# Kernel tuning notes

Measured on AMD Instinct MI355X. Metric: run time of the kernel, lower is better.

The kernel has to match this reference:

```python
import jax, jax.numpy as jnp
import numpy as np

N, E, D, B, C, K, L = 20000, 320000, 256, 16, 2, 6, 3
EPS = 1e-5
BETA, LAM = 0.3, 0.2
ALPHA = 1.0 - BETA - LAM


def setup_inputs() -> dict:
    key = jax.random.key(0)
    ks = jax.random.split(key, 32)
    s = 0.05
    inp = {
        "x": jax.random.normal(ks[0], (N, D), jnp.float32),
        "edge_index": jax.random.randint(ks[1], (2, E), 0, N, jnp.int64) if jax.config.jax_enable_x64 else jax.random.randint(ks[1], (2, E), 0, N, jnp.int32),
        "batch": jnp.sort(jax.random.randint(ks[2], (N,), 0, B, jnp.int32)),
        "labels": jax.random.randint(ks[3], (B,), 0, C, jnp.int32),
        # mask generator MLP: 2D -> 128 -> 64 -> 1
        "mw1": jax.random.normal(ks[4], (128, 2 * D), jnp.float32) * s,
        "mb1": jnp.zeros((128,), jnp.float32),
        "mw2": jax.random.normal(ks[5], (64, 128), jnp.float32) * s,
        "mb2": jnp.zeros((64,), jnp.float32),
        "mw3": jax.random.normal(ks[6], (1, 64), jnp.float32) * s,
        "mb3": jnp.zeros((1,), jnp.float32),
        # frozen CFG encoder: L DGCN layers (W_self, W_in, W_out + BN eval stats)
        "Ws": jax.random.normal(ks[7], (L, D, D), jnp.float32) * s,
        "bs": jnp.zeros((L, D), jnp.float32),
        "Win": jax.random.normal(ks[8], (L, D, D), jnp.float32) * s,
        "bin_": jnp.zeros((L, D), jnp.float32),
        "Wout": jax.random.normal(ks[9], (L, D, D), jnp.float32) * s,
        "bout": jnp.zeros((L, D), jnp.float32),
        "gamma": jnp.ones((L, D), jnp.float32),
        "beta": jnp.zeros((L, D), jnp.float32),
        "rmean": jax.random.normal(ks[10], (L, D), jnp.float32) * s,
        "rvar": jax.random.uniform(ks[11], (L, D), jnp.float32, 0.5, 1.5),
        # semantic anchors and frozen classifier
        "anchors": jax.random.normal(ks[12], (K, D), jnp.float32),
        "Wc": jax.random.normal(ks[13], (C, D), jnp.float32) * s,
        "bc": jnp.zeros((C,), jnp.float32),
    }
    return inp


def _encoder(x0, src, dst, mask, Ws, bs, Win, bin_, Wout, bout, gamma, beta, rmean, rvar):
    """Bidirectional edge-weighted gather/scatter_add message passing, L layers."""
    n = x0.shape[0]
    h = x0
    mcol = mask[:, None]
    for l in range(L):
        agg_in = jax.ops.segment_sum(h[src] * mcol, dst, num_segments=n)   # (N, D)
        agg_out = jax.ops.segment_sum(h[dst] * mcol, src, num_segments=n)  # (N, D)
        h = h @ Ws[l].T + bs[l] + agg_in @ Win[l].T + bin_[l] + agg_out @ Wout[l].T + bout[l]
        h = jax.nn.relu(h)
        h = (h - rmean[l]) * jax.lax.rsqrt(rvar[l] + EPS) * gamma[l] + beta[l]  # BN (eval)
    return h


def _anchor_stat(emb, anchors):
    # sum over anchors of euclidean distance: (B,)
    d = emb[:, None, :] - anchors[None, :, :]
    return jnp.sqrt(jnp.sum(d * d, axis=-1)).sum(axis=-1)


def reference(x, edge_index, batch, labels, mw1, mb1, mw2, mb2, mw3, mb3,
              Ws, bs, Win, bin_, Wout, bout, gamma, beta, rmean, rvar,
              anchors, Wc, bc):
    src, dst = edge_index[0], edge_index[1]
    enc = lambda m: _encoder(x, src, dst, m, Ws, bs, Win, bin_, Wout, bout, gamma, beta, rmean, rvar)

    ones_e = jnp.ones((src.shape[0],), x.dtype)
    node_emb = enc(ones_e)

    # mask generator: z = h_src || h_dst -> MLP -> sigmoid
    z = jnp.concatenate([node_emb[src], node_emb[dst]], axis=-1)  # (E, 2D)
    h1 = jax.nn.relu(z @ mw1.T + mb1)
    h2 = jax.nn.relu(h1 @ mw2.T + mb2)
    mask = jax.nn.sigmoid((h2 @ mw3.T + mb3)[:, 0])               # (E,)

    cnt = jnp.clip(jax.ops.segment_sum(jnp.ones((x.shape[0],), x.dtype), batch, num_segments=B), 1.0)

    def masked_fwd(m):
        h = enc(m)
        gemb = jax.ops.segment_sum(h, batch, num_segments=B) / cnt[:, None]  # mean pool
        return gemb @ Wc.T + bc, gemb

    logits_sub, emb_sub = masked_fwd(mask)
    logits_comp, _ = masked_fwd(1.0 - mask)
    _, orig_emb = masked_fwd(ones_e)
    orig_emb = jax.lax.stop_gradient(orig_emb)  # torch.no_grad() pass

    s_orig = _anchor_stat(orig_emb, anchors)
    s_sub = _anchor_stat(emb_sub, anchors)
    L_align = jnp.mean((s_sub - jax.lax.stop_gradient(s_orig)) ** 2)

    logp = jax.nn.log_softmax(logits_sub, axis=-1)
    L_pred = -jnp.mean(jnp.take_along_axis(logp, labels[:, None].astype(jnp.int32), axis=1)[:, 0])

    p_comp = jax.nn.softmax(logits_comp, axis=-1)
    u = 1.0 / C
    # F.kl_div(log(p+1e-8), uniform, 'batchmean')
    L_uni = jnp.sum(u * (jnp.log(u) - jnp.log(p_comp + 1e-8))) / B

    total = ALPHA * L_pred + BETA * L_uni + LAM * L_align
    return total, L_pred, L_uni, L_align, mask
```

## Files before the change

kernel.cpp:

```cpp
#include <hip/hip_runtime.h>
#include <hip/hip_bf16.h>

constexpr int Nn = 20000;
constexpr int Ee = 320000;
constexpr int Dd = 256;
constexpr int Bb = 16;
constexpr float EPSc = 1e-5f;

using v8s = __attribute__((ext_vector_type(8))) short;
using v4f = __attribute__((ext_vector_type(4))) float;
using v2f = __attribute__((ext_vector_type(2))) float;

__device__ __forceinline__ float b2f(ushort u) { return __uint_as_float(((unsigned)u) << 16); }
__device__ __forceinline__ ushort f2b(float f) {
  __hip_bfloat16 h = __float2bfloat16(f);
  return *reinterpret_cast<ushort*>(&h);
}

#ifndef __has_builtin
#define __has_builtin(x) 0
#endif
#if __has_builtin(__builtin_amdgcn_cvt_pk_f32_fp8) && __has_builtin(__builtin_amdgcn_cvt_pk_fp8_f32)
#define FP8CVT 1
#else
#define FP8CVT 0
#endif

__device__ __forceinline__ unsigned f2fp8(float v) {
#if FP8CVT
  return (unsigned)__builtin_amdgcn_cvt_pk_fp8_f32(v, 0.f, 0, false) & 0xFFu;
#else
  unsigned u = __float_as_uint(v);
  unsigned s = (u >> 24) & 0x80u;
  unsigned a = u & 0x7FFFFFFFu;
  if (a >= 0x43F00000u) return s | 0x7Eu;
  unsigned r = a + 0x0007FFFFu + ((a >> 20) & 1u);
  int e = (int)(r >> 23) - 120;
  if (e <= 0) return s;
  return s | ((unsigned)e << 3) | ((r >> 20) & 7u);
#endif
}

__device__ __forceinline__ void fp8x8_dec(unsigned lo, unsigned hi, float* f) {
#if FP8CVT
  v2f p0 = __builtin_amdgcn_cvt_pk_f32_fp8((int)lo, false);
  v2f p1 = __builtin_amdgcn_cvt_pk_f32_fp8((int)lo, true);
  v2f p2 = __builtin_amdgcn_cvt_pk_f32_fp8((int)hi, false);
  v2f p3 = __builtin_amdgcn_cvt_pk_f32_fp8((int)hi, true);
  f[0] = p0[0]; f[1] = p0[1]; f[2] = p1[0]; f[3] = p1[1];
  f[4] = p2[0]; f[5] = p2[1]; f[6] = p3[0]; f[7] = p3[1];
#else
#pragma unroll
  for (int j = 0; j < 8; ++j) {
    unsigned b = (j < 4) ? ((lo >> (8 * j)) & 0xFFu) : ((hi >> (8 * (j - 4))) & 0xFFu);
    unsigned s = (b & 0x80u) << 24;
    unsigned e = (b >> 3) & 15u, m = b & 7u;
    float x;
    if (e) x = __uint_as_float(s | ((e + 120u) << 23) | (m << 20));
    else { x = (float)(int)m * 0x1p-9f; if (s) x = -x; }
    f[j] = x;
  }
#endif
}

__global__ void hist_edges_k(const int* __restrict__ src, const int* __restrict__ dst,
                             int* __restrict__ cin, int* __restrict__ cout) {
  int e = blockIdx.x * 256 + threadIdx.x;
  if (e < Ee) { atomicAdd(&cin[dst[e]], 1); atomicAdd(&cout[src[e]], 1); }
}

__global__ void cnt_batch_k(const int* __restrict__ batch, float* __restrict__ cntf) {
  int b = threadIdx.x;
  if (b < Bb) {
    int lo = 0, hi = Nn;
    while (lo < hi) { int mid = (lo + hi) >> 1; if (batch[mid] < b) lo = mid + 1; else hi = mid; }
    int lb = lo;
    lo = 0; hi = Nn;
    while (lo < hi) { int mid = (lo + hi) >> 1; if (batch[mid] <= b) lo = mid + 1; else hi = mid; }
    cntf[b] = (float)(lo - lb);
  }
}

__global__ __launch_bounds__(1024) void scan_k(const int* __restrict__ cin,
                                               const int* __restrict__ cout,
                                               int* __restrict__ off_in, int* __restrict__ off_out,
                                               int* __restrict__ cur_in, int* __restrict__ cur_out) {
  __shared__ int part[1024];
  const int tid = threadIdx.x;
  for (int which = 0; which < 2; ++which) {
    const int* cnt = which ? cout : cin;
    int* off = which ? off_out : off_in;
    int* curp = which ? cur_out : cur_in;
    int vals[20];
    int base = tid * 20;
    int local = 0;
#pragma unroll
    for (int i = 0; i < 20; ++i) {
      int idx = base + i;
      int v = (idx < Nn) ? cnt[idx] : 0;
      vals[i] = v; local += v;
    }
    part[tid] = local;
    __syncthreads();
    for (int ofs = 1; ofs < 1024; ofs <<= 1) {
      int t = (tid >= ofs) ? part[tid - ofs] : 0;
      __syncthreads();
      part[tid] += t;
      __syncthreads();
    }
    int run = part[tid] - local;
#pragma unroll
    for (int i = 0; i < 20; ++i) {
      int idx = base + i;
      if (idx < Nn) { off[idx] = run; curp[idx] = run; run += vals[i]; }
    }
    if (tid == 0) off[Nn] = Ee;
    __syncthreads();
  }
}

__global__ void scatter_k(const int* __restrict__ src, const int* __restrict__ dst,
                          int* __restrict__ cur_in, int* __restrict__ cur_out,
                          int* __restrict__ in_src, int* __restrict__ in_eid,
                          int* __restrict__ out_dst, int* __restrict__ out_eid,
                          int* __restrict__ out_srcn) {
  int e = blockIdx.x * 256 + threadIdx.x;
  if (e < Ee) {
    int d = dst[e], s = src[e];
    int p = atomicAdd(&cur_in[d], 1);  in_src[p] = s;  in_eid[p] = e;
    int q = atomicAdd(&cur_out[s], 1); out_dst[q] = d; out_eid[q] = e; out_srcn[q] = s;
  }
}

__global__ void prep_bsum_k(const float* __restrict__ bs, const float* __restrict__ bin,
                            const float* __restrict__ bout, float* __restrict__ bsum) {
  int t = threadIdx.x;
  for (int l = 0; l < 3; ++l) bsum[l * 256 + t] = bs[l * 256 + t] + bin[l * 256 + t] + bout[l * 256 + t];
}

__global__ void copyxb_k(const float* __restrict__ x, ushort* __restrict__ h) {
  const int n4 = Nn * Dd / 4;
  int i = blockIdx.x * 256 + threadIdx.x;
  if (i < n4) {
    float4 v = ((const float4*)x)[i];
    ushort4 o; o.x = f2b(v.x); o.y = f2b(v.y); o.z = f2b(v.z); o.w = f2b(v.w);
    ((ushort4*)h)[i] = o;
  }
}

__global__ void c_f2b_k(const float* __restrict__ s, ushort* __restrict__ d, int n) {
  int i = blockIdx.x * 256 + threadIdx.x;
  if (i < n) d[i] = f2b(s[i]);
}

__global__ void prep_mlp_k(const float* __restrict__ mw1, const float* __restrict__ mb1,
                           const float* __restrict__ mw2,
                           ushort* __restrict__ Wcombb, ushort* __restrict__ W2b,
                           float* __restrict__ bcomb) {
  int i = blockIdx.x * 256 + threadIdx.x;
  if (i < 65536) {
    int r = i >> 8, c = i & 255;
    float v = (r < 128) ? mw1[r * 512 + c] : mw1[(r - 128) * 512 + 256 + c];
    Wcombb[i] = f2b(v);
  }
  if (i < 8192) W2b[i] = f2b(mw2[i]);
  if (i < 256) bcomb[i] = (i < 128) ? mb1[i] : 0.f;
}

__global__ void permmask_k(const float* __restrict__ mask,
                           const int* __restrict__ in_eid, float* __restrict__ minA) {
  int i = blockIdx.x * 256 + threadIdx.x;
  if (i < Ee) minA[i] = mask[in_eid[i]];
}

template <int EMIT8>
__global__ __launch_bounds__(256) void gemm768t_k(
    const ushort* __restrict__ A, const ushort* __restrict__ W0,
    const ushort* __restrict__ W1, const ushort* __restrict__ W2,
    ushort* __restrict__ Y, unsigned char* __restrict__ Y8, int M) {
  __shared__ ushort lds[10240];
  ushort* As = lds;
  ushort* Bs = lds + 5120;
  const int tid = threadIdx.x;
  const int wid = tid >> 6, lane = tid & 63;
  const int wr = wid & 1, wc = wid >> 1;
  const int m0 = blockIdx.x * 128;
  const int by = blockIdx.y;
  const int seg = by >> 1;
  const ushort* Wp = (seg == 0) ? W0 : ((seg == 1) ? W1 : W2);
  const int nb0 = (by & 1) * 128;
  const int lrow = lane & 15;
  const int klo = (lane >> 4) * 8;
  const int r0 = tid >> 2, c80 = (tid & 3) * 8;
  const int r1 = (tid + 256) >> 2, c81 = ((tid + 256) & 3) * 8;
  int ar0 = m0 + r0; if (ar0 >= M) ar0 = M - 1;
  int ar1 = m0 + r1; if (ar1 >= M) ar1 = M - 1;
  v4f acc[4][4] = {};
  for (int kc = 0; kc < 256; kc += 32) {
    __syncthreads();
    *(v8s*)&As[r0 * 40 + c80] = *(const v8s*)(A + (size_t)ar0 * 256 + kc + c80);
    *(v8s*)&As[r1 * 40 + c81] = *(const v8s*)(A + (size_t)ar1 * 256 + kc + c81);
    *(v8s*)&Bs[r0 * 40 + c80] = *(const v8s*)(Wp + (size_t)(nb0 + r0) * 256 + kc + c80);
    *(v8s*)&Bs[r1 * 40 + c81] = *(const v8s*)(Wp + (size_t)(nb0 + r1) * 256 + kc + c81);
    __syncthreads();
    v8s a[4], b[4];
#pragma unroll
    for (int f = 0; f < 4; ++f) {
      a[f] = *(const v8s*)&As[(wr * 64 + f * 16 + lrow) * 40 + klo];
      b[f] = *(const v8s*)&Bs[(wc * 64 + f * 16 + lrow) * 40 + klo];
    }
#pragma unroll
    for (int fi = 0; fi < 4; ++fi)
#pragma unroll
      for (int fj = 0; fj < 4; ++fj)
        acc[fi][fj] = __builtin_amdgcn_mfma_f32_16x16x32_bf16(a[fi], b[fj], acc[fi][fj], 0, 0, 0);
  }
  __syncthreads();
  const int colq = by * 128 + wc * 64;
  if (EMIT8) {
    unsigned char* ep = (unsigned char*)lds + wid * 3072;
#pragma unroll
    for (int hf = 0; hf < 2; ++hf) {
#pragma unroll
      for (int fi = 0; fi < 2; ++fi) {
        const int fI = hf * 2 + fi;
        const int rl0 = fi * 16 + ((lane >> 4) << 2);
#pragma unroll
        for (int fj = 0; fj < 4; ++fj)
#pragma unroll
          for (int r = 0; r < 4; ++r)
            ep[(rl0 + r) * 96 + fj * 16 + lrow] = (unsigned char)f2fp8(acc[fI][fj][r]);
      }
#pragma unroll
      for (int i = 0; i < 2; ++i) {
        const int rl = (lane >> 2) + i * 16;
        const int cb = (lane & 3) * 16;
        uint4 val = *(const uint4*)&ep[rl * 96 + cb];
        const int grow = m0 + wr * 64 + hf * 32 + rl;
        if (grow < M)
          *(uint4*)(Y8 + (size_t)grow * 768 + colq + cb) = val;
      }
    }
  } else {
    ushort* ep = lds + wid * 2304;
#pragma unroll
    for (int hf = 0; hf < 2; ++hf) {
#pragma unroll
      for (int fi = 0; fi < 2; ++fi) {
        const int fI = hf * 2 + fi;
        const int rl0 = fi * 16 + ((lane >> 4) << 2);
#pragma unroll
        for (int fj = 0; fj < 4; ++fj)
#pragma unroll
          for (int r = 0; r < 4; ++r)
            ep[(rl0 + r) * 72 + fj * 16 + lrow] = f2b(acc[fI][fj][r]);
      }
#pragma unroll
      for (int i = 0; i < 4; ++i) {
        const int rl = (lane >> 2) + (i & 1) * 16;
        const int oct = (lane & 3) + (i >> 1) * 4;
        v8s val = *(const v8s*)&ep[rl * 72 + oct * 8];
        const int grow = m0 + wr * 64 + hf * 32 + rl;
        if (grow < M)
          *(v8s*)(Y + (size_t)grow * 768 + colq + oct * 8) = val;
      }
    }
  }
}

template <int MODE, int WR>
__global__ __launch_bounds__(256) void aggepi_k(
    const ushort* __restrict__ Y, ushort* __restrict__ hout, ushort* __restrict__ raw,
    const int* __restrict__ off_in, const int* __restrict__ in_src,
    const int* __restrict__ off_out, const int* __restrict__ out_dst,
    const float* __restrict__ minA, const float* __restrict__ moutA,
    const float* __restrict__ bsum, const float* __restrict__ gma,
    const float* __restrict__ bta, const float* __restrict__ rmn, const float* __restrict__ rvr,
    int Mtot) {
  const int g = threadIdx.x >> 5;
  const int lane = threadIdx.x & 31;
  const int node = blockIdx.x * 8 + g;
  if (node >= Mtot) return;
  const int v = node;
  const int co = lane * 8;
  float acc[8] = {};
#pragma unroll
  for (int dir = 0; dir < 2; ++dir) {
    const int* offs = dir ? off_out : off_in;
    const int* nbr  = dir ? out_dst : in_src;
    const float* ma = dir ? moutA : minA;
    const ushort* Yg = Y + (dir ? 512 : 256) + co;
    const int s = offs[v], e = offs[v + 1];
    int i = s;
    for (; i + 4 <= e; i += 4) {
      int u[4]; float m[4];
#pragma unroll
      for (int t = 0; t < 4; ++t) {
        u[t] = nbr[i + t];
        m[t] = (MODE == 0) ? 1.f : ma[i + t];
      }
      v8s r[4];
#pragma unroll
      for (int t = 0; t < 4; ++t) r[t] = *(const v8s*)(Yg + (size_t)u[t] * 768);
#pragma unroll
      for (int t = 0; t < 4; ++t)
#pragma unroll
        for (int j = 0; j < 8; ++j) acc[j] += m[t] * b2f((ushort)r[t][j]);
    }
    for (; i < e; ++i) {
      int u = nbr[i];
      float m = (MODE == 0) ? 1.f : ma[i];
      v8s r = *(const v8s*)(Yg + (size_t)u * 768);
#pragma unroll
      for (int j = 0; j < 8; ++j) acc[j] += m * b2f((ushort)r[j]);
    }
  }
  if (WR) {
    v8s rw;
#pragma unroll
    for (int j = 0; j < 8; ++j) rw[j] = (short)f2b(acc[j]);
    *(v8s*)(raw + (size_t)v * 256 + co) = rw;
  }
  v8s ys = *(const v8s*)(Y + (size_t)v * 768 + co);
  v8s o;
#pragma unroll
  for (int j = 0; j < 8; ++j) {
    const int col = co + j;
    float val = acc[j] + b2f((ushort)ys[j]) + bsum[col];
    val = fmaxf(val, 0.f);
    val = (val - rmn[col]) * rsqrtf(rvr[col] + EPSc) * gma[col] + bta[col];
    o[j] = (short)f2b(val);
  }
  *(v8s*)(hout + (size_t)node * 256 + co) = o;
}

__global__ __launch_bounds__(256) void aggepi8_k(
    const unsigned char* __restrict__ Y8, ushort* __restrict__ hout,
    const int* __restrict__ off_in, const int* __restrict__ in_src,
    const int* __restrict__ off_out, const int* __restrict__ out_dst,
    const float* __restrict__ minA, const float* __restrict__ moutA,
    const float* __restrict__ bsum, const float* __restrict__ gma,
    const float* __restrict__ bta, const float* __restrict__ rmn, const float* __restrict__ rvr) {
  const int g = threadIdx.x >> 5;
  const int lane = threadIdx.x & 31;
  const int node = blockIdx.x * 8 + g;
  if (node >= 2 * Nn) return;
  const int half = (node >= Nn) ? 1 : 0;
  const int v = node - half * Nn;
  const int co = lane * 8;
  float acc[8] = {};
#pragma unroll
  for (int dir = 0; dir < 2; ++dir) {
    const int* offs = dir ? off_out : off_in;
    const int* nbr  = dir ? out_dst : in_src;
    const float* ma = dir ? moutA : minA;
    const unsigned char* Yg = Y8 + (size_t)half * Nn * 768 + (dir ? 512 : 256) + co;
    const int s = offs[v], e = offs[v + 1];
    int i = s;
    for (; i + 4 <= e; i += 4) {
      int u[4]; float m[4];
#pragma unroll
      for (int t = 0; t < 4; ++t) {
        u[t] = nbr[i + t];
        float mv = ma[i + t];
        m[t] = half ? (1.f - mv) : mv;
      }
      uint2 r[4];
#pragma unroll
      for (int t = 0; t < 4; ++t) r[t] = *(const uint2*)(Yg + (size_t)u[t] * 768);
#pragma unroll
      for (int t = 0; t < 4; ++t) {
        float f[8];
        fp8x8_dec(r[t].x, r[t].y, f);
#pragma unroll
        for (int j = 0; j < 8; ++j) acc[j] += m[t] * f[j];
      }
    }
    for (; i < e; ++i) {
      int u = nbr[i];
      float mv = ma[i];
      float m = half ? (1.f - mv) : mv;
      uint2 r = *(const uint2*)(Yg + (size_t)u * 768);
      float f[8];
      fp8x8_dec(r.x, r.y, f);
#pragma unroll
      for (int j = 0; j < 8; ++j) acc[j] += m * f[j];
    }
  }
  uint2 rs = *(const uint2*)(Y8 + (size_t)(half * Nn + v) * 768 + co);
  float fs[8];
  fp8x8_dec(rs.x, rs.y, fs);
  v8s o;
#pragma unroll
  for (int j = 0; j < 8; ++j) {
    const int col = co + j;
    float val = acc[j] + fs[j] + bsum[col];
    val = fmaxf(val, 0.f);
    val = (val - rmn[col]) * rsqrtf(rvr[col] + EPSc) * gma[col] + bta[col];
    o[j] = (short)f2b(val);
  }
  *(v8s*)(hout + (size_t)node * 256 + co) = o;
}

__global__ void compl0_k(const ushort* __restrict__ Yx, const ushort* __restrict__ Aones,
                         const ushort* __restrict__ Asub, ushort* __restrict__ hout,
                         const float* __restrict__ bsum, const float* __restrict__ gma,
                         const float* __restrict__ bta, const float* __restrict__ rmn,
                         const float* __restrict__ rvr) {
  int i = blockIdx.x * 256 + threadIdx.x;
  if (i >= Nn * 32) return;
  const int v = i >> 5;
  const int co = (i & 31) * 8;
  v8s ys = *(const v8s*)(Yx + (size_t)v * 768 + co);
  v8s ao = *(const v8s*)(Aones + (size_t)v * 256 + co);
  v8s as = *(const v8s*)(Asub + (size_t)v * 256 + co);
  v8s o;
#pragma unroll
  for (int j = 0; j < 8; ++j) {
    const int col = co + j;
    float val = b2f((ushort)ys[j]) + b2f((ushort)ao[j]) - b2f((ushort)as[j]) + bsum[col];
    val = fmaxf(val, 0.f);
    val = (val - rmn[col]) * rsqrtf(rvr[col] + EPSc) * gma[col] + bta[col];
    o[j] = (short)f2b(val);
  }
  *(v8s*)(hout + (size_t)(Nn + v) * 256 + co) = o;
}

template <int EPI>
__global__ __launch_bounds__(256) void mfma_gemm2_k(
    const ushort* __restrict__ A, const ushort* __restrict__ W,
    ushort* __restrict__ Cout, int M, const float* __restrict__ bias) {
  __shared__ ushort eplds[4][32][72];
  const int tid = threadIdx.x;
  const int wid = tid >> 6, lane = tid & 63;
  const int wr = wid & 1, wc = wid >> 1;
  const int m0 = blockIdx.x * 64 + wr * 32;
  const int n0 = blockIdx.y * 128 + wc * 64;
  const int lrow = lane & 15;
  const int klo = (lane >> 4) * 8;
  int rowA[2];
#pragma unroll
  for (int fi = 0; fi < 2; ++fi) {
    int r = m0 + fi * 16 + lrow;
    rowA[fi] = (r < M) ? r : (M - 1);
  }
  v4f acc[2][4] = {};
#pragma unroll
  for (int c = 0; c < 8; ++c) {
    v8s a[2], b[4];
#pragma unroll
    for (int fi = 0; fi < 2; ++fi)
      a[fi] = *(const v8s*)(A + (size_t)rowA[fi] * 256 + c * 32 + klo);
#pragma unroll
    for (int fj = 0; fj < 4; ++fj)
      b[fj] = *(const v8s*)(W + (size_t)(n0 + fj * 16 + lrow) * 256 + c * 32 + klo);
#pragma unroll
    for (int fi = 0; fi < 2; ++fi)
#pragma unroll
      for (int fj = 0; fj < 4; ++fj)
        acc[fi][fj] = __builtin_amdgcn_mfma_f32_16x16x32_bf16(a[fi], b[fj], acc[fi][fj], 0, 0, 0);
  }
#pragma unroll
  for (int fj = 0; fj < 4; ++fj) {
    const int col = n0 + fj * 16 + lrow;
    const float bsv = bias ? bias[col] : 0.f;
#pragma unroll
    for (int fi = 0; fi < 2; ++fi) {
      const int rl0 = fi * 16 + ((lane >> 4) << 2);
#pragma unroll
      for (int r = 0; r < 4; ++r)
        eplds[wid][rl0 + r][fj * 16 + lrow] = f2b(acc[fi][fj][r] + bsv);
    }
  }
#pragma unroll
  for (int i = 0; i < 4; ++i) {
    const int rl = (lane >> 2) + (i & 1) * 16;
    const int oct = (lane & 3) + (i >> 1) * 4;
    v8s val = *(const v8s*)&eplds[wid][rl][oct * 8];
    const int grow = m0 + rl;
    if (grow < M)
      *(v8s*)(Cout + (size_t)grow * 256 + n0 + oct * 8) = val;
  }
}

__global__ __launch_bounds__(256) void edge_mlp4_k(const ushort* __restrict__ P,
                                                   const int* __restrict__ out_srcn,
                                                   const int* __restrict__ out_dst,
                                                   const int* __restrict__ out_eid,
                                                   const ushort* __restrict__ W2b,
                                                   const float* __restrict__ b2, const float* __restrict__ w3,
                                                   const float* __restrict__ b3,
                                                   float* __restrict__ maskOut, float* __restrict__ moutA) {
  const int tid = threadIdx.x;
  const int w = tid >> 6, lane = tid & 63;
  const int e0 = blockIdx.x * 64 + w * 16;
  const int le = lane & 15;
  const int kq = lane >> 4;
  const int klo = kq * 8;
  const int pA = e0 + le;
  const int s_ = out_srcn[pA], d_ = out_dst[pA];
  const ushort* ps = P + (size_t)s_ * 256;
  const ushort* pd = P + (size_t)d_ * 256 + 128;
  v8s as[4], ad[4];
#pragma unroll
  for (int c = 0; c < 4; ++c) {
    as[c] = *(const v8s*)(ps + c * 32 + klo);
    ad[c] = *(const v8s*)(pd + c * 32 + klo);
  }
  v4f acc[4] = {};
#pragma unroll
  for (int c = 0; c < 4; ++c) {
    v8s h;
#pragma unroll
    for (int j = 0; j < 8; ++j) {
      float v = fmaxf(b2f((ushort)as[c][j]) + b2f((ushort)ad[c][j]), 0.f);
      h[j] = (short)f2b(v);
    }
#pragma unroll
    for (int fj = 0; fj < 4; ++fj) {
      v8s b = *(const v8s*)(W2b + (size_t)(fj * 16 + le) * 128 + c * 32 + klo);
      acc[fj] = __builtin_amdgcn_mfma_f32_16x16x32_bf16(h, b, acc[fj], 0, 0, 0);
    }
  }
  float b2v[4], w3v[4];
#pragma unroll
  for (int fj = 0; fj < 4; ++fj) { b2v[fj] = b2[fj * 16 + le]; w3v[fj] = w3[fj * 16 + le]; }
  const float b3v = b3[0];
#pragma unroll
  for (int r = 0; r < 4; ++r) {
    float val = 0.f;
#pragma unroll
    for (int fj = 0; fj < 4; ++fj)
      val += fmaxf(acc[fj][r] + b2v[fj], 0.f) * w3v[fj];
    val += __shfl_xor(val, 1);
    val += __shfl_xor(val, 2);
    val += __shfl_xor(val, 4);
    val += __shfl_xor(val, 8);
    if (le == 0) {
      int pos = e0 + kq * 4 + r;
      float sig = 1.0f / (1.0f + expf(-(val + b3v)));
      moutA[pos] = sig;
      maskOut[out_eid[pos]] = sig;
    }
  }
}

__global__ __launch_bounds__(256) void gemb_sum_k(const ushort* __restrict__ h, const int* __restrict__ batch,
                                                  float* __restrict__ gsum, int batched) {
  const int halfBlocks = Nn / 16;
  int blk = blockIdx.x;
  int half = 0, bi = blk;
  if (batched) { half = (blk >= halfBlocks) ? 1 : 0; bi = blk - half * halfBlocks; }
  const int v0 = bi * 16;
  const int tid = threadIdx.x;
  const size_t base = (size_t)half * Nn;
  float* out = gsum + (size_t)half * (Bb * Dd);
  float acc = 0.0f;
  int curb = batch[v0];
  for (int i = 0; i < 16; ++i) {
    int v = v0 + i;
    int b = batch[v];
    if (b != curb) { atomicAdd(&out[curb * Dd + tid], acc); acc = 0.0f; curb = b; }
    acc += b2f(h[(base + v) * Dd + tid]);
  }
  atomicAdd(&out[curb * Dd + tid], acc);
}

__global__ void gemb_scale_k(float* __restrict__ g, const float* __restrict__ cntf) {
  int blk = blockIdx.x;
  int b = blk & 15;
  g[blk * Dd + threadIdx.x] /= fmaxf(cntf[b], 1.0f);
}

__global__ void anchor_k(const float* __restrict__ g, const float* __restrict__ anchors,
                         float* __restrict__ s_out) {
  __shared__ float red4[4];
  const int b = blockIdx.x, tid = threadIdx.x;
  float gv = g[b * Dd + tid];
  float total = 0.0f;
  for (int k = 0; k < 6; ++k) {
    float d = gv - anchors[k * Dd + tid];
    float v = d * d;
    for (int o = 32; o > 0; o >>= 1) v += __shfl_xor(v, o);
    if ((tid & 63) == 0) red4[tid >> 6] = v;
    __syncthreads();
    if (tid == 0) total += sqrtf(red4[0] + red4[1] + red4[2] + red4[3]);
    __syncthreads();
  }
  if (tid == 0) s_out[b] = total;
}

__global__ void logits_k(const float* __restrict__ gsub, const float* __restrict__ gcomp,
                         const float* __restrict__ Wc, const float* __restrict__ bc,
                         float* __restrict__ outL) {
  __shared__ float red4[4];
  const int blk = blockIdx.x;
  const int set = blk >> 4, b = blk & 15;
  const float* g = set ? gcomp : gsub;
  const int tid = threadIdx.x;
  float gv = g[b * Dd + tid];
  for (int c = 0; c < 2; ++c) {
    float v = gv * Wc[c * Dd + tid];
    for (int o = 32; o > 0; o >>= 1) v += __shfl_xor(v, o);
    if ((tid & 63) == 0) red4[tid >> 6] = v;
    __syncthreads();
    if (tid == 0) outL[set * 32 + b * 2 + c] = red4[0] + red4[1] + red4[2] + red4[3] + bc[c];
    __syncthreads();
  }
}

__global__ void final_k(const float* __restrict__ L, const int* __restrict__ labels,
                        const float* __restrict__ s_orig, const float* __restrict__ s_sub,
                        float* __restrict__ out) {
  if (threadIdx.x == 0) {
    float Lp = 0, Lu = 0, La = 0;
    const float u = 0.5f;
    for (int b = 0; b < 16; ++b) {
      float l0 = L[b * 2], l1 = L[b * 2 + 1];
      float m = fmaxf(l0, l1);
      float lse = m + logf(expf(l0 - m) + expf(l1 - m));
      int lab = labels[b];
      Lp += -((lab ? l1 : l0) - lse);
      float c0 = L[32 + b * 2], c1 = L[32 + b * 2 + 1];
      float mm = fmaxf(c0, c1);
      float e0 = expf(c0 - mm), e1 = expf(c1 - mm), Z = e0 + e1;
      Lu += u * (logf(u) - logf(e0 / Z + 1e-8f)) + u * (logf(u) - logf(e1 / Z + 1e-8f));
      float dd = s_sub[b] - s_orig[b];
      La += dd * dd;
    }
    Lp /= 16.0f; Lu /= 16.0f; La /= 16.0f;
    out[0] = 0.5f * Lp + 0.3f * Lu + 0.2f * La;
    out[1] = Lp; out[2] = Lu; out[3] = La;
  }
}

extern "C" void kernel_launch(void* const* d_in, const int* in_sizes, int n_in,
                              void* d_out, int out_size, void* d_ws, size_t ws_size,
                              hipStream_t stream) {
  (void)in_sizes; (void)n_in; (void)out_size; (void)ws_size;
  const float* x    = (const float*)d_in[0];
  const int* ei     = (const int*)d_in[1];
  const int* batch  = (const int*)d_in[2];
  const int* labels = (const int*)d_in[3];
  const float* mw1 = (const float*)d_in[4];
  const float* mb1 = (const float*)d_in[5];
  const float* mw2 = (const float*)d_in[6];
  const float* mb2 = (const float*)d_in[7];
  const float* mw3 = (const float*)d_in[8];
  const float* mb3 = (const float*)d_in[9];
  const float* Ws   = (const float*)d_in[10];
  const float* bs   = (const float*)d_in[11];
  const float* Win  = (const float*)d_in[12];
  const float* bin_ = (const float*)d_in[13];
  const float* Wout = (const float*)d_in[14];
  const float* bout = (const float*)d_in[15];
  const float* gma  = (const float*)d_in[16];
  const float* bta  = (const float*)d_in[17];
  const float* rmn  = (const float*)d_in[18];
  const float* rvr  = (const float*)d_in[19];
  const float* anchors = (const float*)d_in[20];
  const float* Wc   = (const float*)d_in[21];
  const float* bc   = (const float*)d_in[22];
  const int* srcp = ei;
  const int* dstp = ei + Ee;

  const size_t NH = (size_t)Nn * Dd;
  const size_t NY = (size_t)Nn * 768;
  ushort* xb   = (ushort*)d_ws;
  ushort* hA   = xb + NH;
  ushort* hB   = hA + 2 * NH;
  ushort* Yx   = hB + 2 * NH;
  ushort* Ybuf = Yx + NY;
  ushort* Pb   = Ybuf;
  unsigned char* Y8 = (unsigned char*)Ybuf;
  ushort* Aones = Ybuf + 2 * NY;
  ushort* Asub  = Aones + NH;
  ushort* Wsb   = Asub + NH;
  ushort* Winb  = Wsb + 3 * 65536;
  ushort* Woutb = Winb + 3 * 65536;
  ushort* Wcombb = Woutb + 3 * 65536;
  ushort* W2b    = Wcombb + 65536;
  float* bcomb = (float*)(W2b + 8192);
  float* minA  = bcomb + 256;
  float* moutA = minA + Ee;
  int* off_in   = (int*)(moutA + Ee);
  int* off_out  = off_in + (Nn + 1);
  int* cur_in   = off_out + (Nn + 1);
  int* cur_out  = cur_in + Nn;
  int* in_src   = cur_out + Nn;
  int* in_eid   = in_src + Ee;
  int* out_dst  = in_eid + Ee;
  int* out_eid  = out_dst + Ee;
  int* out_srcn = out_eid + Ee;
  int* counts_in  = out_srcn + Ee;
  int* counts_out = counts_in + Nn;
  float* cntf      = (float*)(counts_out + Nn);
  float* gemb_orig = cntf + Bb;
  float* gemb_sub  = gemb_orig + Bb * Dd;
  float* gemb_comp = gemb_sub + Bb * Dd;
  float* bsum    = gemb_comp + Bb * Dd;
  float* s_orig  = bsum + 3 * Dd;
  float* s_sub   = s_orig + Bb;
  float* logitsb = s_sub + Bb;

  float* outF = (float*)d_out;
  float* maskp = outF + 4;

  const size_t zero_bytes = (char*)bsum - (char*)counts_in;
  hipMemsetAsync(counts_in, 0, zero_bytes, stream);

  hist_edges_k<<<(Ee + 255) / 256, 256, 0, stream>>>(srcp, dstp, counts_in, counts_out);
  cnt_batch_k<<<1, 64, 0, stream>>>(batch, cntf);
  scan_k<<<1, 1024, 0, stream>>>(counts_in, counts_out, off_in, off_out, cur_in, cur_out);
  scatter_k<<<(Ee + 255) / 256, 256, 0, stream>>>(srcp, dstp, cur_in, cur_out, in_src, in_eid,
                                                  out_dst, out_eid, out_srcn);
  prep_bsum_k<<<1, 256, 0, stream>>>(bs, bin_, bout, bsum);

  c_f2b_k<<<(3 * 65536 + 255) / 256, 256, 0, stream>>>(Ws, Wsb, 3 * 65536);
  c_f2b_k<<<(3 * 65536 + 255) / 256, 256, 0, stream>>>(Win, Winb, 3 * 65536);
  c_f2b_k<<<(3 * 65536 + 255) / 256, 256, 0, stream>>>(Wout, Woutb, 3 * 65536);
  prep_mlp_k<<<256, 256, 0, stream>>>(mw1, mb1, mw2, Wcombb, W2b, bcomb);

  auto run_gemm768 = [&](const ushort* h, ushort* Yout, int M, int l) {
    dim3 gg((M + 127) / 128, 6);
    gemm768t_k<0><<<gg, 256, 0, stream>>>(h, Wsb + (size_t)l * 65536, Winb + (size_t)l * 65536,
                                          Woutb + (size_t)l * 65536, Yout, nullptr, M);
  };
  auto run_gemm768_8 = [&](const ushort* h, int M, int l) {
    dim3 gg((M + 127) / 128, 6);
    gemm768t_k<1><<<gg, 256, 0, stream>>>(h, Wsb + (size_t)l * 65536, Winb + (size_t)l * 65536,
                                          Woutb + (size_t)l * 65536, nullptr, Y8, M);
  };
  auto bn = [&](int l) { return bsum + l * 256; };
  const int aggN = (Nn + 7) / 8;
  const int agg2N = (2 * Nn + 7) / 8;

  copyxb_k<<<(Nn * Dd / 4 + 255) / 256, 256, 0, stream>>>(x, xb);
  run_gemm768(xb, Yx, Nn, 0);
  aggepi_k<0, 1><<<aggN, 256, 0, stream>>>(
      Yx, hB, Aones, off_in, in_src, off_out, out_dst, nullptr, nullptr,
      bn(0), gma, bta, rmn, rvr, Nn);
  run_gemm768(hB, Ybuf, Nn, 1);
  aggepi_k<0, 0><<<aggN, 256, 0, stream>>>(
      Ybuf, hA, nullptr, off_in, in_src, off_out, out_dst, nullptr, nullptr,
      bn(1), gma + 256, bta + 256, rmn + 256, rvr + 256, Nn);
  run_gemm768(hA, Ybuf, Nn, 2);
  aggepi_k<0, 0><<<aggN, 256, 0, stream>>>(
      Ybuf, hB, nullptr, off_in, in_src, off_out, out_dst, nullptr, nullptr,
      bn(2), gma + 512, bta + 512, rmn + 512, rvr + 512, Nn);

  gemb_sum_k<<<Nn / 16, 256, 0, stream>>>(hB, batch, gemb_orig, 0);
  gemb_scale_k<<<Bb, 256, 0, stream>>>(gemb_orig, cntf);
  anchor_k<<<Bb, 256, 0, stream>>>(gemb_orig, anchors, s_orig);

  {
    dim3 gp((Nn + 63) / 64, 2);
    mfma_gemm2_k<3><<<gp, 256, 0, stream>>>(hB, Wcombb, Pb, Nn, bcomb);
  }
  edge_mlp4_k<<<Ee / 64, 256, 0, stream>>>(Pb, out_srcn, out_dst, out_eid,
                                           W2b, mb2, mw3, mb3, maskp, moutA);
  permmask_k<<<(Ee + 255) / 256, 256, 0, stream>>>(maskp, in_eid, minA);

  aggepi_k<1, 1><<<aggN, 256, 0, stream>>>(
      Yx, hA, Asub, off_in, in_src, off_out, out_dst, minA, moutA,
      bn(0), gma, bta, rmn, rvr, Nn);
  compl0_k<<<(Nn * 32 + 255) / 256, 256, 0, stream>>>(Yx, Aones, Asub, hA,
                                                      bn(0), gma, bta, rmn, rvr);
  run_gemm768_8(hA, 2 * Nn, 1);
  aggepi8_k<<<agg2N, 256, 0, stream>>>(
      Y8, hB, off_in, in_src, off_out, out_dst, minA, moutA,
      bn(1), gma + 256, bta + 256, rmn + 256, rvr + 256);
  run_gemm768_8(hB, 2 * Nn, 2);
  aggepi8_k<<<agg2N, 256, 0, stream>>>(
      Y8, hA, off_in, in_src, off_out, out_dst, minA, moutA,
      bn(2), gma + 512, bta + 512, rmn + 512, rvr + 512);

  gemb_sum_k<<<2 * (Nn / 16), 256, 0, stream>>>(hA, batch, gemb_sub, 1);
  gemb_scale_k<<<2 * Bb, 256, 0, stream>>>(gemb_sub, cntf);
  anchor_k<<<Bb, 256, 0, stream>>>(gemb_sub, anchors, s_sub);
  logits_k<<<2 * Bb, 256, 0, stream>>>(gemb_sub, gemb_comp, Wc, bc, logitsb);
  final_k<<<1, 64, 0, stream>>>(logitsb, labels, s_orig, s_sub, outF);
}
```

Baseline: 685.8 us.

## Double-buffer LDS tiles in gemm768t and raise priority in edge MLP MFMA loop

The 768-wide GEMM now double-buffers its A/B tiles in LDS. The next k-chunk is loaded into registers before the MFMAs and written to the other buffer afterwards, so each iteration needs one barrier instead of two and global latency overlaps compute. The edge mask MLP kernel also wraps its MFMA loop in s_setprio to favour that wave while it is in the compute phase. LDS use doubles to 40KB per block, which may reduce occupancy.

```diff
diff --git a/kernel.cpp b/kernel.cpp
--- a/kernel.cpp
+++ b/kernel.cpp
@@ -178,9 +178,7 @@
     const ushort* __restrict__ A, const ushort* __restrict__ W0,
     const ushort* __restrict__ W1, const ushort* __restrict__ W2,
     ushort* __restrict__ Y, unsigned char* __restrict__ Y8, int M) {
-  __shared__ ushort lds[10240];
-  ushort* As = lds;
-  ushort* Bs = lds + 5120;
+  __shared__ ushort lds[20480];
   const int tid = threadIdx.x;
   const int wid = tid >> 6, lane = tid & 63;
   const int wr = wid & 1, wc = wid >> 1;
@@ -195,25 +193,49 @@
   const int r1 = (tid + 256) >> 2, c81 = ((tid + 256) & 3) * 8;
   int ar0 = m0 + r0; if (ar0 >= M) ar0 = M - 1;
   int ar1 = m0 + r1; if (ar1 >= M) ar1 = M - 1;
+  const ushort* Ap0 = A + (size_t)ar0 * 256 + c80;
+  const ushort* Ap1 = A + (size_t)ar1 * 256 + c81;
+  const ushort* Wp0 = Wp + (size_t)(nb0 + r0) * 256 + c80;
+  const ushort* Wp1 = Wp + (size_t)(nb0 + r1) * 256 + c81;
+
+  v8s sa0, sa1, sb0, sb1;
+  sa0 = *(const v8s*)(Ap0);  sa1 = *(const v8s*)(Ap1);
+  sb0 = *(const v8s*)(Wp0);  sb1 = *(const v8s*)(Wp1);
+  {
+    ushort* As = lds; ushort* Bs = lds + 5120;
+    *(v8s*)&As[r0 * 40 + c80] = sa0;  *(v8s*)&As[r1 * 40 + c81] = sa1;
+    *(v8s*)&Bs[r0 * 40 + c80] = sb0;  *(v8s*)&Bs[r1 * 40 + c81] = sb1;
+  }
+  __syncthreads();
   v4f acc[4][4] = {};
-  for (int kc = 0; kc < 256; kc += 32) {
-    __syncthreads();
-    *(v8s*)&As[r0 * 40 + c80] = *(const v8s*)(A + (size_t)ar0 * 256 + kc + c80);
-    *(v8s*)&As[r1 * 40 + c81] = *(const v8s*)(A + (size_t)ar1 * 256 + kc + c81);
-    *(v8s*)&Bs[r0 * 40 + c80] = *(const v8s*)(Wp + (size_t)(nb0 + r0) * 256 + kc + c80);
-    *(v8s*)&Bs[r1 * 40 + c81] = *(const v8s*)(Wp + (size_t)(nb0 + r1) * 256 + kc + c81);
-    __syncthreads();
+#pragma unroll
+  for (int it = 0; it < 8; ++it) {
+    const int cur = it & 1;
+    ushort* Asc = lds + cur * 10240;
+    ushort* Bsc = Asc + 5120;
+    if (it < 7) {
+      const int kc = (it + 1) * 32;
+      sa0 = *(const v8s*)(Ap0 + kc);  sa1 = *(const v8s*)(Ap1 + kc);
+      sb0 = *(const v8s*)(Wp0 + kc);  sb1 = *(const v8s*)(Wp1 + kc);
+    }
     v8s a[4], b[4];
 #pragma unroll
     for (int f = 0; f < 4; ++f) {
-      a[f] = *(const v8s*)&As[(wr * 64 + f * 16 + lrow) * 40 + klo];
-      b[f] = *(const v8s*)&Bs[(wc * 64 + f * 16 + lrow) * 40 + klo];
+      a[f] = *(const v8s*)&Asc[(wr * 64 + f * 16 + lrow) * 40 + klo];
+      b[f] = *(const v8s*)&Bsc[(wc * 64 + f * 16 + lrow) * 40 + klo];
     }
 #pragma unroll
     for (int fi = 0; fi < 4; ++fi)
 #pragma unroll
       for (int fj = 0; fj < 4; ++fj)
         acc[fi][fj] = __builtin_amdgcn_mfma_f32_16x16x32_bf16(a[fi], b[fj], acc[fi][fj], 0, 0, 0);
+    if (it < 7) {
+      ushort* Asn = lds + (cur ^ 1) * 10240;
+      ushort* Bsn = Asn + 5120;
+      *(v8s*)&Asn[r0 * 40 + c80] = sa0;  *(v8s*)&Asn[r1 * 40 + c81] = sa1;
+      *(v8s*)&Bsn[r0 * 40 + c80] = sb0;  *(v8s*)&Bsn[r1 * 40 + c81] = sb1;
+      __syncthreads();
+    }
   }
   __syncthreads();
   const int colq = by * 128 + wc * 64;
@@ -508,6 +530,7 @@
     ad[c] = *(const v8s*)(pd + c * 32 + klo);
   }
   v4f acc[4] = {};
+  __builtin_amdgcn_s_setprio(1);
 #pragma unroll
   for (int c = 0; c < 4; ++c) {
     v8s h;
@@ -522,6 +545,7 @@
       acc[fj] = __builtin_amdgcn_mfma_f32_16x16x32_bf16(h, b, acc[fj], 0, 0, 0);
     }
   }
+  __builtin_amdgcn_s_setprio(0);
   float b2v[4], w3v[4];
 #pragma unroll
   for (int fj = 0; fj < 4; ++fj) { b2v[fj] = b2[fj * 16 + le]; w3v[fj] = w3[fj * 16 + le]; }
```

After: 691.3 us. About the same (+0.8%).
